# Kernel optimization log

Measured on AMD Instinct MI355X. Metric: run time of the kernel, lower is better.

The kernel has to match this reference:

```python
import jax, jax.numpy as jnp
import numpy as np

B = 2048          # batch
K = 32            # max active features per side
NF = 22528        # feature_set.num_features
L1 = 2048
L2 = 16
L3 = 32
P = 8             # num_psqt_buckets
NLS = 8           # num_ls_buckets
QP = 255.0        # 8-bit unsigned LSQ upper bound


def setup_inputs() -> dict:
    key = jax.random.key(0)
    ks = jax.random.split(key, 16)
    us = jax.random.bernoulli(ks[0], 0.5, (B, 1)).astype(jnp.float32)
    them = 1.0 - us
    white_indices = jax.random.randint(ks[1], (B, K), 0, NF)
    black_indices = jax.random.randint(ks[2], (B, K), 0, NF)
    white_values = jnp.ones((B, K), jnp.float32)
    black_values = jnp.ones((B, K), jnp.float32)
    psqt_indices = jax.random.randint(ks[3], (B,), 0, P)
    layer_stack_indices = jax.random.randint(ks[4], (B,), 0, NLS)
    # parameters
    ft_weight = jax.random.normal(ks[5], (NF, L1 + P), jnp.float32) * 0.01
    ft_bias = jax.random.normal(ks[6], (L1 + P,), jnp.float32) * 0.01
    lsq_s = jnp.full((4,), 1.0 / 128.0, jnp.float32)  # per-group step size
    W1 = jax.random.normal(ks[7], (NLS, L2, L1), jnp.float32) * (1.0 / np.sqrt(L1))
    b1 = jnp.zeros((NLS, L2), jnp.float32)
    W2 = jax.random.normal(ks[8], (NLS, L3, L2), jnp.float32) * (1.0 / np.sqrt(L2))
    b2 = jnp.zeros((NLS, L3), jnp.float32)
    Wo = jax.random.normal(ks[9], (NLS, 1, L3), jnp.float32) * (1.0 / np.sqrt(L3))
    bo = jnp.zeros((NLS, 1), jnp.float32)
    return dict(us=us, them=them, white_indices=white_indices, white_values=white_values,
                black_indices=black_indices, black_values=black_values,
                psqt_indices=psqt_indices, layer_stack_indices=layer_stack_indices,
                ft_weight=ft_weight, ft_bias=ft_bias, lsq_s=lsq_s,
                W1=W1, b1=b1, W2=W2, b2=b2, Wo=Wo, bo=bo)


def _feature_transform(idx, val, ft_weight, ft_bias):
    # sparse accumulation: sum_k val[b,k] * ft_weight[idx[b,k], :]
    emb = ft_weight[idx]                           # [B, K, L1+P]
    return jnp.einsum('bk,bkd->bd', val, emb) + ft_bias


def _lsq(x, s):
    # LSQ activation, 4 groups over feature dim, 8-bit unsigned, STE round
    b, d = x.shape
    g = x.reshape(b, 4, d // 4) / s[None, :, None]
    gc = jnp.clip(g, 0.0, QP)
    gq = gc + jax.lax.stop_gradient(jnp.round(gc) - gc)
    return (gq * s[None, :, None]).reshape(b, d)


def reference(us, them, white_indices, white_values, black_indices, black_values,
              psqt_indices, layer_stack_indices,
              ft_weight, ft_bias, lsq_s, W1, b1, W2, b2, Wo, bo):
    wp = _feature_transform(white_indices, white_values, ft_weight, ft_bias)
    bp = _feature_transform(black_indices, black_values, ft_weight, ft_bias)
    w, wpsqt = wp[:, :L1], wp[:, L1:]
    b, bpsqt = bp[:, :L1], bp[:, L1:]
    l0 = us * jnp.concatenate([w, b], axis=1) + them * jnp.concatenate([b, w], axis=1)
    l0q = _lsq(l0, lsq_s)                          # [B, 2*L1]
    s0, s1, s2, s3 = jnp.split(l0q, 4, axis=1)
    l0_mixed = jnp.concatenate([s0 * s1, s2 * s3], axis=1)   # [B, L1]
    # psqt bucket gather
    wps = jnp.take_along_axis(wpsqt, psqt_indices[:, None], axis=1)  # [B,1]
    bps = jnp.take_along_axis(bpsqt, psqt_indices[:, None], axis=1)
    # per-sample layer-stack (expert) selection
    i = layer_stack_indices
    h1 = jnp.clip(jnp.einsum('bi,boi->bo', l0_mixed, W1[i]) + b1[i], 0.0, 1.0)
    h2 = jnp.clip(jnp.einsum('bi,boi->bo', h1, W2[i]) + b2[i], 0.0, 1.0)
    ls_out = jnp.einsum('bi,boi->bo', h2, Wo[i]) + bo[i]     # [B,1]
    return ls_out + (wps - bps) * (us - 0.5)
```

## Files before the change

### kernel.cpp

```cpp
#include <hip/hip_runtime.h>

#define BB 2048
#define K 32
#define ROW 2056
#define L1D 2048

__device__ __forceinline__ void fma4(float4& a, float v, const float4 t) {
    a.x = fmaf(v, t.x, a.x); a.y = fmaf(v, t.y, a.y);
    a.z = fmaf(v, t.z, a.z); a.w = fmaf(v, t.w, a.w);
}

__device__ __forceinline__ float4 add4(float4 a, float4 b) {
    float4 r; r.x = a.x + b.x; r.y = a.y + b.y; r.z = a.z + b.z; r.w = a.w + b.w;
    return r;
}

__device__ __forceinline__ float4 mix4(float ua, float4 a, float ub, float4 b) {
    float4 r;
    r.x = ua * a.x + ub * b.x; r.y = ua * a.y + ub * b.y;
    r.z = ua * a.z + ub * b.z; r.w = ua * a.w + ub * b.w;
    return r;
}

__device__ __forceinline__ float lsq1(float g, float s) {
    return rintf(fminf(fmaxf(g / s, 0.f), 255.f)) * s;
}

__device__ __forceinline__ float4 lsq4(float4 g, float s) {
    float4 r;
    r.x = lsq1(g.x, s); r.y = lsq1(g.y, s); r.z = lsq1(g.z, s); r.w = lsq1(g.w, s);
    return r;
}

__global__ __launch_bounds__(256) void nnue_fwd(
    const float* __restrict__ us_p,
    const float* __restrict__ them_p,
    const int*   __restrict__ widx,
    const float* __restrict__ wval,
    const int*   __restrict__ bidx,
    const float* __restrict__ bval,
    const int*   __restrict__ psqt_idx,
    const int*   __restrict__ ls_idx,
    const float* __restrict__ ftw,
    const float* __restrict__ ftb,
    const float* __restrict__ lsq_s,
    const float* __restrict__ W1,
    const float* __restrict__ b1,
    const float* __restrict__ W2,
    const float* __restrict__ b2,
    const float* __restrict__ Wo,
    const float* __restrict__ bo,
    float* __restrict__ out)
{
    const int b    = blockIdx.x;
    const int tid  = threadIdx.x;
    const int lane = tid & 63;
    const int wave = tid >> 6;

    __shared__ int   sWI[K], sBI[K];
    __shared__ float sWV[K], sBV[K];
    __shared__ float sM[L1D];
    __shared__ float sPs[16];
    __shared__ float sRed[4][16];
    __shared__ float sH1[16];
    __shared__ float sH2[32];

    if (tid < K) {
        sWI[tid] = widx[b * K + tid];
        sWV[tid] = wval[b * K + tid];
        sBI[tid] = bidx[b * K + tid];
        sBV[tid] = bval[b * K + tid];
    }
    __syncthreads();

    const float usv = us_p[b];
    const float thv = them_p[b];

    float4 aw0 = {0,0,0,0}, aw1 = {0,0,0,0};
    float4 ab0 = {0,0,0,0}, ab1 = {0,0,0,0};

    #pragma unroll 4
    for (int k = 0; k < K; ++k) {
        const float4* rw = (const float4*)(ftw + (size_t)sWI[k] * ROW);
        const float4* rb = (const float4*)(ftw + (size_t)sBI[k] * ROW);
        const float vw = sWV[k];
        const float vb = sBV[k];
        fma4(aw0, vw, rw[tid]);
        fma4(aw1, vw, rw[tid + 256]);
        fma4(ab0, vb, rb[tid]);
        fma4(ab1, vb, rb[tid + 256]);
    }

    if (tid < 4) {
        const int side = tid >> 1;
        const int d4   = 512 + (tid & 1);
        const int*   idx = side ? sBI : sWI;
        const float* val = side ? sBV : sWV;
        float4 acc = {0,0,0,0};
        for (int k = 0; k < K; ++k) {
            const float4* r = (const float4*)(ftw + (size_t)idx[k] * ROW);
            fma4(acc, val[k], r[d4]);
        }
        acc = add4(acc, ((const float4*)ftb)[d4]);
        ((float4*)sPs)[tid] = acc;
    }

    const float4 bl = ((const float4*)ftb)[tid];
    const float4 bh = ((const float4*)ftb)[tid + 256];
    aw0 = add4(aw0, bl); aw1 = add4(aw1, bh);
    ab0 = add4(ab0, bl); ab1 = add4(ab1, bh);

    const float s0 = lsq_s[0], s1 = lsq_s[1], s2 = lsq_s[2], s3 = lsq_s[3];
    const float4 q0 = lsq4(mix4(usv, aw0, thv, ab0), s0);
    const float4 q1 = lsq4(mix4(usv, aw1, thv, ab1), s1);
    const float4 q2 = lsq4(mix4(usv, ab0, thv, aw0), s2);
    const float4 q3 = lsq4(mix4(usv, ab1, thv, aw1), s3);

    float4 mlo, mhi;
    mlo.x = q0.x * q1.x; mlo.y = q0.y * q1.y; mlo.z = q0.z * q1.z; mlo.w = q0.w * q1.w;
    mhi.x = q2.x * q3.x; mhi.y = q2.y * q3.y; mhi.z = q2.z * q3.z; mhi.w = q2.w * q3.w;

    ((float4*)sM)[tid]       = mlo;
    ((float4*)sM)[tid + 256] = mhi;
    __syncthreads();

    const int i = ls_idx[b];
    const float* W1i = W1 + (size_t)i * 16 * L1D;

    float acc[16];
    #pragma unroll
    for (int o = 0; o < 16; ++o) acc[o] = 0.f;

    #pragma unroll
    for (int jj = 0; jj < 8; ++jj) {
        const int j = tid + 256 * jj;
        const float m = sM[j];
        #pragma unroll
        for (int o = 0; o < 16; ++o)
            acc[o] = fmaf(m, W1i[o * L1D + j], acc[o]);
    }

    #pragma unroll
    for (int o = 0; o < 16; ++o) {
        float v = acc[o];
        v += __shfl_down(v, 32); v += __shfl_down(v, 16); v += __shfl_down(v, 8);
        v += __shfl_down(v, 4);  v += __shfl_down(v, 2);  v += __shfl_down(v, 1);
        if (lane == 0) sRed[wave][o] = v;
    }
    __syncthreads();

    if (tid < 16) {
        float v = sRed[0][tid] + sRed[1][tid] + sRed[2][tid] + sRed[3][tid];
        v += b1[i * 16 + tid];
        sH1[tid] = fminf(fmaxf(v, 0.f), 1.f);
    }
    __syncthreads();

    if (tid < 32) {
        const float* W2i = W2 + (size_t)i * 32 * 16 + tid * 16;
        float v = b2[i * 32 + tid];
        #pragma unroll
        for (int j = 0; j < 16; ++j) v = fmaf(sH1[j], W2i[j], v);
        sH2[tid] = fminf(fmaxf(v, 0.f), 1.f);
    }
    __syncthreads();

    if (tid == 0) {
        const float* Woi = Wo + (size_t)i * 32;
        float v = bo[i];
        #pragma unroll
        for (int j = 0; j < 32; ++j) v = fmaf(sH2[j], Woi[j], v);
        const int pi = psqt_idx[b];
        const float wps = sPs[pi];
        const float bps = sPs[8 + pi];
        out[b] = v + (wps - bps) * (usv - 0.5f);
    }
}

extern "C" void kernel_launch(void* const* d_in, const int* in_sizes, int n_in,
                              void* d_out, int out_size, void* d_ws, size_t ws_size,
                              hipStream_t stream) {
    const float* us_p  = (const float*)d_in[0];
    const float* them  = (const float*)d_in[1];
    const int*   widx  = (const int*)d_in[2];
    const float* wval  = (const float*)d_in[3];
    const int*   bidx  = (const int*)d_in[4];
    const float* bval  = (const float*)d_in[5];
    const int*   pidx  = (const int*)d_in[6];
    const int*   lidx  = (const int*)d_in[7];
    const float* ftw   = (const float*)d_in[8];
    const float* ftb   = (const float*)d_in[9];
    const float* lsqs  = (const float*)d_in[10];
    const float* W1    = (const float*)d_in[11];
    const float* b1    = (const float*)d_in[12];
    const float* W2    = (const float*)d_in[13];
    const float* b2    = (const float*)d_in[14];
    const float* Wo    = (const float*)d_in[15];
    const float* bo    = (const float*)d_in[16];
    float* out = (float*)d_out;

    nnue_fwd<<<dim3(BB), dim3(256), 0, stream>>>(
        us_p, them, widx, wval, bidx, bval, pidx, lidx,
        ftw, ftb, lsqs, W1, b1, W2, b2, Wo, bo, out);
}
```

Measured before the change: 398.3 us.

## Widen blocks to 512 threads and restructure the psqt gather and W1 reduction

Doubles the threads per sample, so each thread gathers one float4 per feature row instead of two, and index and value loads come straight from global memory instead of being staged in shared memory. The psqt term is now computed only for the selected bucket, using a 64-lane shuffle reduction; the bias drops out because it cancels in the white-minus-black difference. The first dense layer gives each 32-lane group one output row with coalesced float4 weight loads, instead of every thread accumulating all 16 outputs. The aim is more in-flight gather loads and cheaper W1 reads, at the cost of an extra shared-memory pass and barrier for the pairwise product.

```diff
diff --git a/kernel.cpp b/kernel.cpp
--- a/kernel.cpp
+++ b/kernel.cpp
@@ -4,6 +4,7 @@
 #define K 32
 #define ROW 2056
 #define L1D 2048
+#define NT 512
 
 __device__ __forceinline__ void fma4(float4& a, float v, const float4 t) {
     a.x = fmaf(v, t.x, a.x); a.y = fmaf(v, t.y, a.y);
@@ -17,8 +18,8 @@
 
 __device__ __forceinline__ float4 mix4(float ua, float4 a, float ub, float4 b) {
     float4 r;
-    r.x = ua * a.x + ub * b.x; r.y = ua * a.y + ub * b.y;
-    r.z = ua * a.z + ub * b.z; r.w = ua * a.w + ub * b.w;
+    r.x = fmaf(ua, a.x, ub * b.x); r.y = fmaf(ua, a.y, ub * b.y);
+    r.z = fmaf(ua, a.z, ub * b.z); r.w = fmaf(ua, a.w, ub * b.w);
     return r;
 }
 
@@ -32,7 +33,12 @@
     return r;
 }
 
-__global__ __launch_bounds__(256) void nnue_fwd(
+__device__ __forceinline__ float4 mul4(float4 a, float4 b) {
+    float4 r; r.x = a.x * b.x; r.y = a.y * b.y; r.z = a.z * b.z; r.w = a.w * b.w;
+    return r;
+}
+
+__global__ __launch_bounds__(NT, 8) void nnue_fwd(
     const float* __restrict__ us_p,
     const float* __restrict__ them_p,
     const int*   __restrict__ widx,
@@ -52,128 +58,106 @@
     const float* __restrict__ bo,
     float* __restrict__ out)
 {
-    const int b    = blockIdx.x;
-    const int tid  = threadIdx.x;
-    const int lane = tid & 63;
-    const int wave = tid >> 6;
+    const int b = blockIdx.x;
+    const int t = threadIdx.x;
 
-    __shared__ int   sWI[K], sBI[K];
-    __shared__ float sWV[K], sBV[K];
-    __shared__ float sM[L1D];
-    __shared__ float sPs[16];
-    __shared__ float sRed[4][16];
-    __shared__ float sH1[16];
-    __shared__ float sH2[32];
-
-    if (tid < K) {
-        sWI[tid] = widx[b * K + tid];
-        sWV[tid] = wval[b * K + tid];
-        sBI[tid] = bidx[b * K + tid];
-        sBV[tid] = bval[b * K + tid];
-    }
-    __syncthreads();
+    __shared__ float4 sQA[NT];
+    __shared__ float4 sQB[NT];
+    __shared__ float4 sM[NT];
+    __shared__ float  sH1t[16];
+    __shared__ float  sH1[16];
+    __shared__ float  sH2[32];
+    __shared__ float  sPsq;
 
     const float usv = us_p[b];
     const float thv = them_p[b];
 
-    float4 aw0 = {0,0,0,0}, aw1 = {0,0,0,0};
-    float4 ab0 = {0,0,0,0}, ab1 = {0,0,0,0};
-
+    float4 aw = {0,0,0,0}, ab = {0,0,0,0};
     #pragma unroll 4
     for (int k = 0; k < K; ++k) {
-        const float4* rw = (const float4*)(ftw + (size_t)sWI[k] * ROW);
-        const float4* rb = (const float4*)(ftw + (size_t)sBI[k] * ROW);
-        const float vw = sWV[k];
-        const float vb = sBV[k];
-        fma4(aw0, vw, rw[tid]);
-        fma4(aw1, vw, rw[tid + 256]);
-        fma4(ab0, vb, rb[tid]);
-        fma4(ab1, vb, rb[tid + 256]);
+        const int   iw = widx[b * K + k];
+        const float vw = wval[b * K + k];
+        const int   ib = bidx[b * K + k];
+        const float vb = bval[b * K + k];
+        const float4* rw = (const float4*)(ftw + (size_t)iw * ROW);
+        const float4* rb = (const float4*)(ftw + (size_t)ib * ROW);
+        fma4(aw, vw, rw[t]);
+        fma4(ab, vb, rb[t]);
     }
 
-    if (tid < 4) {
-        const int side = tid >> 1;
-        const int d4   = 512 + (tid & 1);
-        const int*   idx = side ? sBI : sWI;
-        const float* val = side ? sBV : sWV;
-        float4 acc = {0,0,0,0};
-        for (int k = 0; k < K; ++k) {
-            const float4* r = (const float4*)(ftw + (size_t)idx[k] * ROW);
-            fma4(acc, val[k], r[d4]);
-        }
-        acc = add4(acc, ((const float4*)ftb)[d4]);
-        ((float4*)sPs)[tid] = acc;
+    const int pi = psqt_idx[b];
+    if (t < 64) {
+        const int k = t & 31;
+        const int   idx = (t < 32) ? widx[b * K + k] : bidx[b * K + k];
+        const float val = (t < 32) ? wval[b * K + k] : bval[b * K + k];
+        float c = val * ftw[(size_t)idx * ROW + 2048 + pi];
+        c += __shfl_down(c, 16, 32); c += __shfl_down(c, 8, 32);
+        c += __shfl_down(c, 4, 32);  c += __shfl_down(c, 2, 32);
+        c += __shfl_down(c, 1, 32);
+        const float bsum = __shfl(c, 32);
+        if (t == 0) sPsq = (c - bsum) * (usv - 0.5f);
     }
 
-    const float4 bl = ((const float4*)ftb)[tid];
-    const float4 bh = ((const float4*)ftb)[tid + 256];
-    aw0 = add4(aw0, bl); aw1 = add4(aw1, bh);
-    ab0 = add4(ab0, bl); ab1 = add4(ab1, bh);
+    const float s0 = lsq_s[0], s1 = lsq_s[1], s2 = lsq_s[2], s3 = lsq_s[3];
+    const float4 bias = ((const float4*)ftb)[t];
+    aw = add4(aw, bias);
+    ab = add4(ab, bias);
+    const float sA = (t < 256) ? s0 : s1;
+    const float sB = (t < 256) ? s2 : s3;
+    sQA[t] = lsq4(mix4(usv, aw, thv, ab), sA);
+    sQB[t] = lsq4(mix4(usv, ab, thv, aw), sB);
+    __syncthreads();
 
-    const float s0 = lsq_s[0], s1 = lsq_s[1], s2 = lsq_s[2], s3 = lsq_s[3];
-    const float4 q0 = lsq4(mix4(usv, aw0, thv, ab0), s0);
-    const float4 q1 = lsq4(mix4(usv, aw1, thv, ab1), s1);
-    const float4 q2 = lsq4(mix4(usv, ab0, thv, aw0), s2);
-    const float4 q3 = lsq4(mix4(usv, ab1, thv, aw1), s3);
-
-    float4 mlo, mhi;
-    mlo.x = q0.x * q1.x; mlo.y = q0.y * q1.y; mlo.z = q0.z * q1.z; mlo.w = q0.w * q1.w;
-    mhi.x = q2.x * q3.x; mhi.y = q2.y * q3.y; mhi.z = q2.z * q3.z; mhi.w = q2.w * q3.w;
-
-    ((float4*)sM)[tid]       = mlo;
-    ((float4*)sM)[tid + 256] = mhi;
+    if (t < 256) {
+        sM[t]       = mul4(sQA[t], sQA[t + 256]);
+        sM[t + 256] = mul4(sQB[t], sQB[t + 256]);
+    }
     __syncthreads();
 
     const int i = ls_idx[b];
     const float* W1i = W1 + (size_t)i * 16 * L1D;
-
-    float acc[16];
-    #pragma unroll
-    for (int o = 0; o < 16; ++o) acc[o] = 0.f;
-
-    #pragma unroll
-    for (int jj = 0; jj < 8; ++jj) {
-        const int j = tid + 256 * jj;
-        const float m = sM[j];
+    {
+        const int o   = t >> 5;
+        const int sub = t & 31;
+        const float4* Wrow = (const float4*)(W1i + o * L1D);
+        float4 a4 = {0,0,0,0};
         #pragma unroll
-        for (int o = 0; o < 16; ++o)
-            acc[o] = fmaf(m, W1i[o * L1D + j], acc[o]);
-    }
-
-    #pragma unroll
-    for (int o = 0; o < 16; ++o) {
-        float v = acc[o];
-        v += __shfl_down(v, 32); v += __shfl_down(v, 16); v += __shfl_down(v, 8);
-        v += __shfl_down(v, 4);  v += __shfl_down(v, 2);  v += __shfl_down(v, 1);
-        if (lane == 0) sRed[wave][o] = v;
+        for (int jj = 0; jj < 16; ++jj) {
+            const int j4 = sub + (jj << 5);
+            const float4 m = sM[j4];
+            const float4 w = Wrow[j4];
+            a4.x = fmaf(m.x, w.x, a4.x); a4.y = fmaf(m.y, w.y, a4.y);
+            a4.z = fmaf(m.z, w.z, a4.z); a4.w = fmaf(m.w, w.w, a4.w);
+        }
+        float acc = (a4.x + a4.y) + (a4.z + a4.w);
+        acc += __shfl_down(acc, 16, 32); acc += __shfl_down(acc, 8, 32);
+        acc += __shfl_down(acc, 4, 32);  acc += __shfl_down(acc, 2, 32);
+        acc += __shfl_down(acc, 1, 32);
+        if (sub == 0) sH1t[o] = acc;
     }
     __syncthreads();
 
-    if (tid < 16) {
-        float v = sRed[0][tid] + sRed[1][tid] + sRed[2][tid] + sRed[3][tid];
-        v += b1[i * 16 + tid];
-        sH1[tid] = fminf(fmaxf(v, 0.f), 1.f);
+    if (t < 16) {
+        const float v = sH1t[t] + b1[i * 16 + t];
+        sH1[t] = fminf(fmaxf(v, 0.f), 1.f);
     }
     __syncthreads();
 
-    if (tid < 32) {
-        const float* W2i = W2 + (size_t)i * 32 * 16 + tid * 16;
-        float v = b2[i * 32 + tid];
+    if (t < 32) {
+        const float* W2i = W2 + (size_t)i * 32 * 16 + t * 16;
+        float v = b2[i * 32 + t];
         #pragma unroll
         for (int j = 0; j < 16; ++j) v = fmaf(sH1[j], W2i[j], v);
-        sH2[tid] = fminf(fmaxf(v, 0.f), 1.f);
+        sH2[t] = fminf(fmaxf(v, 0.f), 1.f);
     }
     __syncthreads();
 
-    if (tid == 0) {
+    if (t == 0) {
         const float* Woi = Wo + (size_t)i * 32;
         float v = bo[i];
         #pragma unroll
         for (int j = 0; j < 32; ++j) v = fmaf(sH2[j], Woi[j], v);
-        const int pi = psqt_idx[b];
-        const float wps = sPs[pi];
-        const float bps = sPs[8 + pi];
-        out[b] = v + (wps - bps) * (usv - 0.5f);
+        out[b] = v + sPsq;
     }
 }
 
@@ -199,7 +183,7 @@
     const float* bo    = (const float*)d_in[16];
     float* out = (float*)d_out;
 
-    nnue_fwd<<<dim3(BB), dim3(256), 0, stream>>>(
+    nnue_fwd<<<dim3(BB), dim3(NT), 0, stream>>>(
         us_p, them, widx, wval, bidx, bval, pidx, lidx,
         ftw, ftb, lsqs, W1, b1, W2, b2, Wo, bo, out);
 }
```

Result: no change. 396.5 us (-0.5%).
